# Kernel optimization log

Hardware: AMD Instinct MI355X
Metric: run time of the kernel (lower is better)

The kernel has to match this reference:

```python
import jax, jax.numpy as jnp
import numpy as np

N_CLASSES = 256
N_AUDIO_CHANS = 1
N_CHANS = 128
N_RES = 128
N_SKIP = 256
N_END = 256
KERNEL = 2
N_LAYERS = 10
N_STACKS = 3
DILATIONS = [2 ** i for _ in range(N_STACKS) for i in range(N_LAYERS)]
L = len(DILATIONS)
DN = ('NCW', 'OIW', 'NCW')


def setup_inputs() -> dict:
    key = jax.random.key(0)
    ks = jax.random.split(key, 16)
    s = 0.05  # small init keeps 30-layer residual stack numerically tame
    inp = {
        'x': jax.random.normal(ks[0], (4, N_AUDIO_CHANS, 16384), jnp.float32),
        'w_shift': jax.random.normal(ks[1], (N_CHANS, N_AUDIO_CHANS, KERNEL), jnp.float32) * s,
        'b_shift': jnp.zeros((N_CHANS,), jnp.float32),
        'conv_w': jax.random.normal(ks[2], (L, 2 * N_RES, N_CHANS, KERNEL), jnp.float32) * s,
        'conv_b': jnp.zeros((L, 2 * N_RES), jnp.float32),
        'res_w': jax.random.normal(ks[3], (L, N_CHANS, N_RES), jnp.float32) * s,
        'res_b': jnp.zeros((L, N_CHANS), jnp.float32),
        'skip_w': jax.random.normal(ks[4], (L, N_SKIP, N_RES), jnp.float32) * s,
        'skip_b': jnp.zeros((L, N_SKIP), jnp.float32),
        'a_w': jax.random.normal(ks[5], (N_END, N_SKIP), jnp.float32) * s,
        'a_b': jnp.zeros((N_END,), jnp.float32),
        'b_w': jax.random.normal(ks[6], (N_CLASSES * N_AUDIO_CHANS, N_END), jnp.float32) * s,
        'b_b': jnp.zeros((N_CLASSES * N_AUDIO_CHANS,), jnp.float32),
    }
    return inp


def _causal_conv(x, w, b, dilation):
    # left-pad by (k-1)*dilation so outputs depend only on past/present
    pad = (w.shape[-1] - 1) * dilation
    xp = jnp.pad(x, ((0, 0), (0, 0), (pad, 0)))
    y = jax.lax.conv_general_dilated(xp, w, window_strides=(1,), padding='VALID',
                                     rhs_dilation=(dilation,), dimension_numbers=DN)
    return y + b[None, :, None]


def reference(x, w_shift, b_shift, conv_w, conv_b, res_w, res_b,
              skip_w, skip_b, a_w, a_b, b_w, b_b):
    N, C, W = x.shape
    # shifted conv: shift input right by one (prepend 0, drop last), then causal conv
    xs = jnp.pad(x, ((0, 0), (0, 0), (1, 0)))[:, :, :-1]
    h = _causal_conv(xs, w_shift, b_shift, 1)  # (N, n_chans, W)

    skips = jnp.zeros((N, N_SKIP, W), h.dtype)
    for l in range(L):
        g = _causal_conv(h, conv_w[l], conv_b[l], DILATIONS[l])  # (N, 2*res, W)
        a, b_gate = jnp.split(g, 2, axis=1)
        gated = a * jax.nn.sigmoid(b_gate)                        # GLU, (N, res, W)
        h = jnp.einsum('or,nrw->now', res_w[l], gated) + res_b[l][None, :, None] + h
        skips = skips + jnp.einsum('or,nrw->now', skip_w[l], gated) + skip_b[l][None, :, None]

    z = jax.nn.relu(skips)
    z = jax.nn.relu(jnp.einsum('os,nsw->now', a_w, z) + a_b[None, :, None])
    logits = jnp.einsum('oe,new->now', b_w, z) + b_b[None, :, None]
    return logits.reshape(N, N_CLASSES, N_AUDIO_CHANS, W)
```

## Files before the change

### kernel.cpp

```cpp
#include <hip/hip_runtime.h>
#include <math.h>


#define NB 4
#define WLEN 16384
#define C 128
#define S 256
#define NLAYERS 30
#define TT 64
#define NTB (WLEN / TT)
#define XROW 264
#define GROW 136
#define HW 128

typedef _Float16 half8 __attribute__((ext_vector_type(8)));
typedef _Float16 half4 __attribute__((ext_vector_type(4)));
typedef float floatx4 __attribute__((ext_vector_type(4)));

__device__ __forceinline__ float sigmoidf_(float v) {
    return 1.0f / (1.0f + __expf(-v));
}

__global__ void prep_kernel(const float* __restrict__ conv_w,
                            const float* __restrict__ res_w,
                            const float* __restrict__ skip_w,
                            const float* __restrict__ a_w,
                            const float* __restrict__ b_w,
                            const float* __restrict__ conv_b,
                            const float* __restrict__ skip_b,
                            _Float16* __restrict__ cw,
                            _Float16* __restrict__ rsw,
                            _Float16* __restrict__ skw,
                            _Float16* __restrict__ aw,
                            _Float16* __restrict__ bw,
                            float* __restrict__ cbp,
                            float* __restrict__ ssum) {
    const int ncw = NLAYERS * 256 * 256;
    const int nrs = NLAYERS * 128 * 128;
    const int nsk = NLAYERS * 256 * 128;
    const int nab = 256 * 256;
    const int ncb = NLAYERS * 256;
    const int total = ncw + nrs + nsk + nab + nab + ncb + 256;
    for (int idx = blockIdx.x * blockDim.x + threadIdx.x; idx < total;
         idx += gridDim.x * blockDim.x) {
        int i = idx;
        if (i < ncw) {
            int j = i & 7, lane = (i >> 3) & 63, rest = i >> 9;
            int ks = rest & 7; rest >>= 3;
            int mt = rest & 15; int l = rest >> 4;
            int mp = mt * 16 + (lane & 15);
            int orow = (mp >> 1) + (mp & 1) * 128;
            int k = ks * 32 + (lane >> 4) * 8 + j;
            int tap = k >> 7, c = k & 127;
            cw[i] = (_Float16)conv_w[(((size_t)l * 256 + orow) * 128 + c) * 2 + tap];
        } else if (i < ncw + nrs) {
            i -= ncw;
            int j = i & 7, lane = (i >> 3) & 63, rest = i >> 9;
            int ks = rest & 3; rest >>= 2;
            int mt = rest & 7; int l = rest >> 3;
            int m = mt * 16 + (lane & 15);
            int k = ks * 32 + (lane >> 4) * 8 + j;
            rsw[i] = (_Float16)res_w[((size_t)l * 128 + m) * 128 + k];
        } else if (i < ncw + nrs + nsk) {
            i -= ncw + nrs;
            int j = i & 7, lane = (i >> 3) & 63, rest = i >> 9;
            int ks = rest & 3; rest >>= 2;
            int mt = rest & 15; int l = rest >> 4;
            int m = mt * 16 + (lane & 15);
            int k = ks * 32 + (lane >> 4) * 8 + j;
            skw[i] = (_Float16)skip_w[((size_t)l * 256 + m) * 128 + k];
        } else if (i < ncw + nrs + nsk + nab) {
            i -= ncw + nrs + nsk;
            int j = i & 7, lane = (i >> 3) & 63, rest = i >> 9;
            int ks = rest & 7; int mt = rest >> 3;
            aw[i] = (_Float16)a_w[(mt * 16 + (lane & 15)) * 256 + ks * 32 + (lane >> 4) * 8 + j];
        } else if (i < ncw + nrs + nsk + 2 * nab) {
            i -= ncw + nrs + nsk + nab;
            int j = i & 7, lane = (i >> 3) & 63, rest = i >> 9;
            int ks = rest & 7; int mt = rest >> 3;
            bw[i] = (_Float16)b_w[(mt * 16 + (lane & 15)) * 256 + ks * 32 + (lane >> 4) * 8 + j];
        } else if (i < ncw + nrs + nsk + 2 * nab + ncb) {
            i -= ncw + nrs + nsk + 2 * nab;
            int mp = i & 255; int l = i >> 8;
            cbp[i] = conv_b[l * 256 + (mp >> 1) + (mp & 1) * 128];
        } else {
            i -= ncw + nrs + nsk + 2 * nab + ncb;
            float s = 0.f;
            for (int l = 0; l < NLAYERS; ++l) s += skip_b[l * 256 + i];
            ssum[i] = s;
        }
    }
}

__global__ void front_kernel(const float* __restrict__ x,
                             const float* __restrict__ w_shift,
                             const float* __restrict__ b_shift,
                             _Float16* __restrict__ h) {
    const int n = blockIdx.y;
    const int t = blockIdx.x * 256 + threadIdx.x;
    float x1 = (t >= 1) ? x[n * WLEN + t - 1] : 0.0f;
    float x2 = (t >= 2) ? x[n * WLEN + t - 2] : 0.0f;
    _Float16* hq = h + ((size_t)n * WLEN + t) * 128;
    #pragma unroll
    for (int c0 = 0; c0 < 128; c0 += 8) {
        half8 v;
        #pragma unroll
        for (int j = 0; j < 8; ++j) {
            int c = c0 + j;
            v[j] = (_Float16)fmaf(w_shift[2 * c], x2,
                                  fmaf(w_shift[2 * c + 1], x1, b_shift[c]));
        }
        *(half8*)&hq[c0] = v;
    }
}

template <bool FIRST>
__global__ __launch_bounds__(512, 4) void stack_kernel(
    const _Float16* __restrict__ h_in, _Float16* __restrict__ h_out,
    _Float16* __restrict__ chunk,
    const _Float16* __restrict__ cw0, const float* __restrict__ cb0,
    const _Float16* __restrict__ rsw0, const float* __restrict__ rb0,
    const _Float16* __restrict__ skw0, const float* __restrict__ ssum) {
    __shared__ _Float16 SMEM[2 * HW * GROW];
    _Float16* H = SMEM;
    _Float16* G = SMEM + HW * GROW;
    const int n = blockIdx.y, tb = blockIdx.x, t0 = tb * TT;
    const int tid = threadIdx.x;
    const int wave = __builtin_amdgcn_readfirstlane(tid >> 6);
    const int lane = tid & 63, q = lane >> 4, ml = lane & 15;

    floatx4 sacc[2][4];
    if (FIRST) {
        #pragma unroll
        for (int mt = 0; mt < 2; ++mt)
            #pragma unroll
            for (int r = 0; r < 4; ++r) {
                float bias = ssum[32 * wave + mt * 16 + q * 4 + r];
                #pragma unroll
                for (int nt = 0; nt < 4; ++nt) sacc[mt][nt][r] = bias;
            }
    } else {
        const _Float16* cp = chunk + ((size_t)n * NTB + tb) * 16384;
        #pragma unroll
        for (int mt = 0; mt < 2; ++mt)
            #pragma unroll
            for (int nt = 0; nt < 4; ++nt) {
                size_t o = (size_t)((((wave * 2 + mt) * 4) + nt) * 64 + lane) * 4;
                half4 v = *(const half4*)&cp[o];
                #pragma unroll
                for (int r = 0; r < 4; ++r) sacc[mt][nt][r] = (float)v[r];
            }
    }

    const _Float16* hn = h_in + (size_t)n * WLEN * 128;
    #pragma unroll
    for (int it = 0; it < 4; ++it) {
        int idx = it * 512 + tid;
        int seg = idx & 15;
        int w = idx >> 4;
        int src_t = t0 - 64 + w;
        half8 v = (half8)(_Float16)0.0f;
        if (src_t >= 0)
            v = *(const half8*)&hn[(size_t)src_t * 128 + seg * 8];
        *(half8*)&H[w * GROW + seg * 8] = v;
    }
    __syncthreads();

    const _Float16* cw  = cw0;
    const float*    cb  = cb0;
    const _Float16* rsw = rsw0;
    const float*    rb  = rb0;
    const _Float16* skw = skw0;

    #pragma clang loop unroll(disable)
    for (int j = 0; j < 6; ++j) {
        const int d = 1 << j;

        #pragma unroll
        for (int np = 0; np < 2; ++np) {
            floatx4 acc[2][4];
            #pragma unroll
            for (int mt = 0; mt < 2; ++mt)
                #pragma unroll
                for (int r = 0; r < 4; ++r) {
                    float bias = cb[32 * wave + mt * 16 + q * 4 + r];
                    #pragma unroll
                    for (int nt = 0; nt < 4; ++nt) acc[mt][nt][r] = bias;
                }
            #pragma unroll
            for (int hp = 0; hp < 2; ++hp) {
                for (int ks = 0; ks < 4; ++ks) {
                    half8 a[2];
                    #pragma unroll
                    for (int mt = 0; mt < 2; ++mt)
                        a[mt] = *(const half8*)&cw[((((2 * wave + mt) * 8) + hp * 4 + ks) * 64 + lane) * 8];
                    #pragma unroll
                    for (int nt = 0; nt < 4; ++nt) {
                        int row = np * 64 + nt * 16 + ml;
                        if (!hp) { row -= d; if (row < 0) row = 0; }
                        half8 b = *(const half8*)&H[row * GROW + ks * 32 + q * 8];
                        #pragma unroll
                        for (int mt = 0; mt < 2; ++mt)
                            acc[mt][nt] = __builtin_amdgcn_mfma_f32_16x16x32_f16(a[mt], b, acc[mt][nt], 0, 0, 0);
                    }
                }
            }
            #pragma unroll
            for (int mt = 0; mt < 2; ++mt)
                #pragma unroll
                for (int nt = 0; nt < 4; ++nt) {
                    float g0 = acc[mt][nt][0] * sigmoidf_(acc[mt][nt][1]);
                    float g1 = acc[mt][nt][2] * sigmoidf_(acc[mt][nt][3]);
                    _Float16 p[2] = {(_Float16)g0, (_Float16)g1};
                    *(uint32_t*)&G[(np * 64 + nt * 16 + ml) * GROW + 16 * wave + mt * 8 + 2 * q] = *(uint32_t*)p;
                }
        }
        __syncthreads();

        #pragma unroll
        for (int ks = 0; ks < 4; ++ks) {
            half8 a[2];
            #pragma unroll
            for (int mt = 0; mt < 2; ++mt)
                a[mt] = *(const half8*)&skw[((((2 * wave + mt) * 4) + ks) * 64 + lane) * 8];
            #pragma unroll
            for (int nt = 0; nt < 4; ++nt) {
                half8 b = *(const half8*)&G[(64 + nt * 16 + ml) * GROW + ks * 32 + q * 8];
                #pragma unroll
                for (int mt = 0; mt < 2; ++mt)
                    sacc[mt][nt] = __builtin_amdgcn_mfma_f32_16x16x32_f16(a[mt], b, sacc[mt][nt], 0, 0, 0);
            }
        }

        #pragma unroll
        for (int np = 0; np < 2; ++np) {
            floatx4 racc[4];
            #pragma unroll
            for (int r = 0; r < 4; ++r) {
                float bias = rb[16 * wave + q * 4 + r];
                #pragma unroll
                for (int nt = 0; nt < 4; ++nt) racc[nt][r] = bias;
            }
            #pragma unroll
            for (int ks = 0; ks < 4; ++ks) {
                half8 a = *(const half8*)&rsw[(((wave * 4) + ks) * 64 + lane) * 8];
                #pragma unroll
                for (int nt = 0; nt < 4; ++nt) {
                    half8 b = *(const half8*)&G[(np * 64 + nt * 16 + ml) * GROW + ks * 32 + q * 8];
                    racc[nt] = __builtin_amdgcn_mfma_f32_16x16x32_f16(a, b, racc[nt], 0, 0, 0);
                }
            }
            #pragma unroll
            for (int nt = 0; nt < 4; ++nt) {
                int w = np * 64 + nt * 16 + ml;
                int c = 16 * wave + q * 4;
                half4 hv = *(const half4*)&H[w * GROW + c];
                half4 o;
                #pragma unroll
                for (int r = 0; r < 4; ++r)
                    o[r] = (_Float16)(racc[nt][r] + (float)hv[r]);
                *(half4*)&H[w * GROW + c] = o;
            }
        }
        __syncthreads();

        cw  += 65536; cb += 256; rsw += 16384; rb += 128; skw += 32768;
    }

    _Float16* ho = h_out + (size_t)n * WLEN * 128;
    #pragma unroll
    for (int it = 0; it < 2; ++it) {
        int idx = it * 512 + tid;
        int seg = idx & 15;
        int w64 = idx >> 4;
        *(half8*)&ho[(size_t)(t0 + w64) * 128 + seg * 8] =
            *(const half8*)&H[(64 + w64) * GROW + seg * 8];
    }

    {
        _Float16* cp = chunk + ((size_t)n * NTB + tb) * 16384;
        #pragma unroll
        for (int mt = 0; mt < 2; ++mt)
            #pragma unroll
            for (int nt = 0; nt < 4; ++nt) {
                size_t o = (size_t)((((wave * 2 + mt) * 4) + nt) * 64 + lane) * 4;
                half4 v;
                #pragma unroll
                for (int r = 0; r < 4; ++r) v[r] = (_Float16)sacc[mt][nt][r];
                *(half4*)&cp[o] = v;
            }
    }
}

__global__ __launch_bounds__(512, 8) void layer_kernel(
    const _Float16* __restrict__ h_in, _Float16* __restrict__ h_out,
    _Float16* __restrict__ chunk,
    const _Float16* __restrict__ cw, const float* __restrict__ cb,
    const _Float16* __restrict__ rsw, const float* __restrict__ rb,
    const _Float16* __restrict__ skw, int d) {
    __shared__ _Float16 SMEM[2 * TT * GROW];
    _Float16* X0 = SMEM;
    _Float16* X1 = SMEM + TT * GROW;
    _Float16* G  = X0;
    const int n = blockIdx.y, tb = blockIdx.x, t0 = tb * TT;
    const int tid = threadIdx.x;
    const int wave = __builtin_amdgcn_readfirstlane(tid >> 6);
    const int lane = tid & 63, q = lane >> 4, ml = lane & 15;

    const _Float16* hn = h_in + (size_t)n * WLEN * 128;
    #pragma unroll
    for (int it = 0; it < 4; ++it) {
        int idx = it * 512 + tid;
        int seg = idx & 15;
        int rowc = (idx >> 4) & 63;
        int tap = idx >> 10;
        int src_t = t0 + rowc - (tap ? 0 : d);
        half8 v = (half8)(_Float16)0.0f;
        if (src_t >= 0)
            v = *(const half8*)&hn[(size_t)src_t * 128 + seg * 8];
        _Float16* Xb = tap ? X1 : X0;
        *(half8*)&Xb[rowc * GROW + seg * 8] = v;
    }
    __syncthreads();

    floatx4 acc[2][4];
    #pragma unroll
    for (int mt = 0; mt < 2; ++mt)
        #pragma unroll
        for (int r = 0; r < 4; ++r) {
            float bias = cb[32 * wave + mt * 16 + q * 4 + r];
            #pragma unroll
            for (int nt = 0; nt < 4; ++nt) acc[mt][nt][r] = bias;
        }
    #pragma unroll
    for (int hp = 0; hp < 2; ++hp) {
        const _Float16* Xb = hp ? X1 : X0;
        for (int ks = 0; ks < 4; ++ks) {
            half8 a[2];
            #pragma unroll
            for (int mt = 0; mt < 2; ++mt)
                a[mt] = *(const half8*)&cw[((((2 * wave + mt) * 8) + hp * 4 + ks) * 64 + lane) * 8];
            #pragma unroll
            for (int nt = 0; nt < 4; ++nt) {
                half8 b = *(const half8*)&Xb[(nt * 16 + ml) * GROW + ks * 32 + q * 8];
                #pragma unroll
                for (int mt = 0; mt < 2; ++mt)
                    acc[mt][nt] = __builtin_amdgcn_mfma_f32_16x16x32_f16(a[mt], b, acc[mt][nt], 0, 0, 0);
            }
        }
    }
    __syncthreads();

    #pragma unroll
    for (int mt = 0; mt < 2; ++mt)
        #pragma unroll
        for (int nt = 0; nt < 4; ++nt) {
            float g0 = acc[mt][nt][0] * sigmoidf_(acc[mt][nt][1]);
            float g1 = acc[mt][nt][2] * sigmoidf_(acc[mt][nt][3]);
            _Float16 p[2] = {(_Float16)g0, (_Float16)g1};
            *(uint32_t*)&G[(nt * 16 + ml) * GROW + 16 * wave + mt * 8 + 2 * q] = *(uint32_t*)p;
        }
    __syncthreads();

    {
        floatx4 sacc[2][4];
        #pragma unroll
        for (int mt = 0; mt < 2; ++mt)
            #pragma unroll
            for (int nt = 0; nt < 4; ++nt)
                #pragma unroll
                for (int r = 0; r < 4; ++r) sacc[mt][nt][r] = 0.0f;
        #pragma unroll
        for (int ks = 0; ks < 4; ++ks) {
            half8 a[2];
            #pragma unroll
            for (int mt = 0; mt < 2; ++mt)
                a[mt] = *(const half8*)&skw[((((2 * wave + mt) * 4) + ks) * 64 + lane) * 8];
            #pragma unroll
            for (int nt = 0; nt < 4; ++nt) {
                half8 b = *(const half8*)&G[(nt * 16 + ml) * GROW + ks * 32 + q * 8];
                #pragma unroll
                for (int mt = 0; mt < 2; ++mt)
                    sacc[mt][nt] = __builtin_amdgcn_mfma_f32_16x16x32_f16(a[mt], b, sacc[mt][nt], 0, 0, 0);
            }
        }
        _Float16* cp = chunk + ((size_t)n * NTB + tb) * 16384;
        #pragma unroll
        for (int mt = 0; mt < 2; ++mt)
            #pragma unroll
            for (int nt = 0; nt < 4; ++nt) {
                size_t o = (size_t)((((wave * 2 + mt) * 4) + nt) * 64 + lane) * 4;
                half4 v = *(const half4*)&cp[o];
                half4 w;
                #pragma unroll
                for (int r = 0; r < 4; ++r)
                    w[r] = (_Float16)(sacc[mt][nt][r] + (float)v[r]);
                *(half4*)&cp[o] = w;
            }
    }

    {
        floatx4 racc[4];
        #pragma unroll
        for (int r = 0; r < 4; ++r) {
            float bias = rb[16 * wave + q * 4 + r];
            #pragma unroll
            for (int nt = 0; nt < 4; ++nt) racc[nt][r] = bias;
        }
        #pragma unroll
        for (int ks = 0; ks < 4; ++ks) {
            half8 a = *(const half8*)&rsw[(((wave * 4) + ks) * 64 + lane) * 8];
            #pragma unroll
            for (int nt = 0; nt < 4; ++nt) {
                half8 b = *(const half8*)&G[(nt * 16 + ml) * GROW + ks * 32 + q * 8];
                racc[nt] = __builtin_amdgcn_mfma_f32_16x16x32_f16(a, b, racc[nt], 0, 0, 0);
            }
        }
        _Float16* ho = h_out + (size_t)n * WLEN * 128;
        #pragma unroll
        for (int nt = 0; nt < 4; ++nt) {
            int tt = nt * 16 + ml;
            int c = 16 * wave + q * 4;
            half4 hv = *(const half4*)&X1[tt * GROW + c];
            half4 o;
            #pragma unroll
            for (int r = 0; r < 4; ++r)
                o[r] = (_Float16)(racc[nt][r] + (float)hv[r]);
            *(half4*)&ho[(size_t)(t0 + tt) * 128 + c] = o;
        }
    }
}

__global__ __launch_bounds__(512, 8) void head_kernel(
    float* __restrict__ out, const _Float16* __restrict__ chunk,
    const _Float16* __restrict__ aw, const float* __restrict__ ab,
    const _Float16* __restrict__ bw, const float* __restrict__ bb) {
    __shared__ _Float16 X[TT * XROW];
    const int n = blockIdx.y, tb = blockIdx.x, t0 = tb * TT;
    const int tid = threadIdx.x;
    const int wave = __builtin_amdgcn_readfirstlane(tid >> 6);
    const int lane = tid & 63, q = lane >> 4, ml = lane & 15;

    {
        const _Float16* cp = chunk + ((size_t)n * NTB + tb) * 16384;
        #pragma unroll
        for (int mt = 0; mt < 2; ++mt)
            #pragma unroll
            for (int nt = 0; nt < 4; ++nt) {
                size_t o = (size_t)((((wave * 2 + mt) * 4) + nt) * 64 + lane) * 4;
                half4 v = *(const half4*)&cp[o];
                half4 z;
                #pragma unroll
                for (int r = 0; r < 4; ++r)
                    z[r] = (_Float16)fmaxf((float)v[r], 0.0f);
                *(half4*)&X[(nt * 16 + ml) * XROW + 32 * wave + mt * 16 + q * 4] = z;
            }
    }
    __syncthreads();

    floatx4 acc[2][4];
    #pragma unroll
    for (int mt = 0; mt < 2; ++mt)
        #pragma unroll
        for (int r = 0; r < 4; ++r) {
            float bias = ab[32 * wave + mt * 16 + q * 4 + r];
            #pragma unroll
            for (int nt = 0; nt < 4; ++nt) acc[mt][nt][r] = bias;
        }
    for (int ks = 0; ks < 8; ++ks) {
        half8 a[2];
        #pragma unroll
        for (int mt = 0; mt < 2; ++mt)
            a[mt] = *(const half8*)&aw[((((2 * wave + mt) * 8) + ks) * 64 + lane) * 8];
        #pragma unroll
        for (int nt = 0; nt < 4; ++nt) {
            half8 b = *(const half8*)&X[(nt * 16 + ml) * XROW + ks * 32 + q * 8];
            #pragma unroll
            for (int mt = 0; mt < 2; ++mt)
                acc[mt][nt] = __builtin_amdgcn_mfma_f32_16x16x32_f16(a[mt], b, acc[mt][nt], 0, 0, 0);
        }
    }
    __syncthreads();
    #pragma unroll
    for (int mt = 0; mt < 2; ++mt)
        #pragma unroll
        for (int nt = 0; nt < 4; ++nt) {
            half4 z;
            #pragma unroll
            for (int r = 0; r < 4; ++r)
                z[r] = (_Float16)fmaxf(acc[mt][nt][r], 0.0f);
            *(half4*)&X[(nt * 16 + ml) * XROW + 32 * wave + mt * 16 + q * 4] = z;
        }
    __syncthreads();

    #pragma unroll
    for (int mt = 0; mt < 2; ++mt)
        #pragma unroll
        for (int r = 0; r < 4; ++r) {
            float bias = bb[32 * wave + mt * 16 + q * 4 + r];
            #pragma unroll
            for (int nt = 0; nt < 4; ++nt) acc[mt][nt][r] = bias;
        }
    for (int ks = 0; ks < 8; ++ks) {
        half8 a[2];
        #pragma unroll
        for (int mt = 0; mt < 2; ++mt)
            a[mt] = *(const half8*)&bw[((((2 * wave + mt) * 8) + ks) * 64 + lane) * 8];
        #pragma unroll
        for (int nt = 0; nt < 4; ++nt) {
            half8 b = *(const half8*)&X[(nt * 16 + ml) * XROW + ks * 32 + q * 8];
            #pragma unroll
            for (int mt = 0; mt < 2; ++mt)
                acc[mt][nt] = __builtin_amdgcn_mfma_f32_16x16x32_f16(a[mt], b, acc[mt][nt], 0, 0, 0);
        }
    }
    float* on = out + (size_t)n * S * WLEN;
    #pragma unroll
    for (int mt = 0; mt < 2; ++mt)
        #pragma unroll
        for (int nt = 0; nt < 4; ++nt)
            #pragma unroll
            for (int r = 0; r < 4; ++r) {
                int o = 32 * wave + mt * 16 + q * 4 + r;
                int tt = t0 + nt * 16 + ml;
                on[(size_t)o * WLEN + tt] = acc[mt][nt][r];
            }
}

extern "C" void kernel_launch(void* const* d_in, const int* in_sizes, int n_in,
                              void* d_out, int out_size, void* d_ws, size_t ws_size,
                              hipStream_t stream) {
    (void)in_sizes; (void)n_in; (void)out_size; (void)ws_size;
    const float* x       = (const float*)d_in[0];
    const float* w_shift = (const float*)d_in[1];
    const float* b_shift = (const float*)d_in[2];
    const float* conv_w  = (const float*)d_in[3];
    const float* conv_b  = (const float*)d_in[4];
    const float* res_w   = (const float*)d_in[5];
    const float* res_b   = (const float*)d_in[6];
    const float* skip_w  = (const float*)d_in[7];
    const float* skip_b  = (const float*)d_in[8];
    const float* a_w     = (const float*)d_in[9];
    const float* a_b     = (const float*)d_in[10];
    const float* b_w     = (const float*)d_in[11];
    const float* b_b     = (const float*)d_in[12];
    float* out = (float*)d_out;

    char* ws = (char*)d_ws;
    size_t off = 0;
    _Float16* hA    = (_Float16*)(ws + off); off += (size_t)NB * WLEN * 128 * 2;
    _Float16* hB    = (_Float16*)(ws + off); off += (size_t)NB * WLEN * 128 * 2;
    _Float16* chunk = (_Float16*)(ws + off); off += (size_t)NB * NTB * 16384 * 2;
    _Float16* cw  = (_Float16*)(ws + off); off += (size_t)NLAYERS * 256 * 256 * 2;
    _Float16* rsw = (_Float16*)(ws + off); off += (size_t)NLAYERS * 128 * 128 * 2;
    _Float16* skw = (_Float16*)(ws + off); off += (size_t)NLAYERS * 256 * 128 * 2;
    _Float16* aw  = (_Float16*)(ws + off); off += 256 * 256 * 2;
    _Float16* bw  = (_Float16*)(ws + off); off += 256 * 256 * 2;
    float* cbp  = (float*)(ws + off); off += (size_t)NLAYERS * 256 * 4;
    float* ssum = (float*)(ws + off); off += 256 * 4;

    prep_kernel<<<512, 256, 0, stream>>>(conv_w, res_w, skip_w, a_w, b_w,
                                         conv_b, skip_b,
                                         cw, rsw, skw, aw, bw, cbp, ssum);
    front_kernel<<<dim3(WLEN / 256, NB), 256, 0, stream>>>(x, w_shift, b_shift, hA);

    const dim3 grid(NTB, NB);
    _Float16* hin = hA;
    _Float16* hout = hB;
    for (int s = 0; s < 3; ++s) {
        const int l0 = s * 10;
        if (s == 0)
            stack_kernel<true><<<grid, 512, 0, stream>>>(
                hin, hout, chunk,
                cw + (size_t)l0 * 65536, cbp + l0 * 256,
                rsw + (size_t)l0 * 16384, res_b + l0 * 128,
                skw + (size_t)l0 * 32768, ssum);
        else
            stack_kernel<false><<<grid, 512, 0, stream>>>(
                hin, hout, chunk,
                cw + (size_t)l0 * 65536, cbp + l0 * 256,
                rsw + (size_t)l0 * 16384, res_b + l0 * 128,
                skw + (size_t)l0 * 32768, ssum);
        { _Float16* tmp = hin; hin = hout; hout = tmp; }
        for (int jj = 6; jj < 10; ++jj) {
            const int l = l0 + jj;
            const int dil = 1 << jj;
            layer_kernel<<<grid, 512, 0, stream>>>(
                hin, hout, chunk,
                cw + (size_t)l * 65536, cbp + l * 256,
                rsw + (size_t)l * 16384, res_b + l * 128,
                skw + (size_t)l * 32768, dil);
            _Float16* tmp = hin; hin = hout; hout = tmp;
        }
    }

    head_kernel<<<grid, 512, 0, stream>>>(out, chunk, aw, a_b, bw, b_b);
}
```

Baseline: 1.099 ms.

## Split fused stack kernel into two with tight halos and XOR-swizzled LDS

The fused first-six-layer kernel is split into two templated kernels. One runs layers with dilations 1–8 using a 16-step halo; the other runs dilations 16–32 using a 48-step halo. Both replace the old uniform 64-step halo, which cut redundant recomputation of overlap rows per tile. LDS rows are now XOR-swizzled instead of padded, and launch bounds are raised so smaller shared-memory tiles allow more resident blocks. In exchange there is an extra kernel launch plus one more round trip of the hidden state and skip chunk through global memory.

```diff
diff --git a/kernel.cpp b/kernel.cpp
--- a/kernel.cpp
+++ b/kernel.cpp
@@ -11,7 +11,8 @@
 #define NTB (WLEN / TT)
 #define XROW 264
 #define GROW 136
-#define HW 128
+
+#define SX(row, c) ((row) * 128 + ((c) ^ (((row) & 7) << 3)))
 
 typedef _Float16 half8 __attribute__((ext_vector_type(8)));
 typedef _Float16 half4 __attribute__((ext_vector_type(4)));
@@ -114,16 +115,17 @@
     }
 }
 
-template <bool FIRST>
-__global__ __launch_bounds__(512, 4) void stack_kernel(
+template <int E0, int NL, int NT, int HALO, bool FIRST>
+__global__ __launch_bounds__(512, 8) void stack_kernel(
     const _Float16* __restrict__ h_in, _Float16* __restrict__ h_out,
     _Float16* __restrict__ chunk,
     const _Float16* __restrict__ cw0, const float* __restrict__ cb0,
     const _Float16* __restrict__ rsw0, const float* __restrict__ rb0,
     const _Float16* __restrict__ skw0, const float* __restrict__ ssum) {
-    __shared__ _Float16 SMEM[2 * HW * GROW];
+    constexpr int WR = NT * 16;
+    __shared__ _Float16 SMEM[2 * WR * 128];
     _Float16* H = SMEM;
-    _Float16* G = SMEM + HW * GROW;
+    _Float16* G = SMEM + WR * 128;
     const int n = blockIdx.y, tb = blockIdx.x, t0 = tb * TT;
     const int tid = threadIdx.x;
     const int wave = __builtin_amdgcn_readfirstlane(tid >> 6);
@@ -154,15 +156,17 @@
 
     const _Float16* hn = h_in + (size_t)n * WLEN * 128;
     #pragma unroll
-    for (int it = 0; it < 4; ++it) {
+    for (int it = 0; it < (WR * 16 + 511) / 512; ++it) {
         int idx = it * 512 + tid;
-        int seg = idx & 15;
-        int w = idx >> 4;
-        int src_t = t0 - 64 + w;
-        half8 v = (half8)(_Float16)0.0f;
-        if (src_t >= 0)
-            v = *(const half8*)&hn[(size_t)src_t * 128 + seg * 8];
-        *(half8*)&H[w * GROW + seg * 8] = v;
+        if (idx < WR * 16) {
+            int seg = idx & 15;
+            int w = idx >> 4;
+            int src_t = t0 - HALO + w;
+            half8 v = (half8)(_Float16)0.0f;
+            if (src_t >= 0)
+                v = *(const half8*)&hn[(size_t)src_t * 128 + seg * 8];
+            *(half8*)&H[SX(w, seg * 8)] = v;
+        }
     }
     __syncthreads();
 
@@ -173,11 +177,11 @@
     const _Float16* skw = skw0;
 
     #pragma clang loop unroll(disable)
-    for (int j = 0; j < 6; ++j) {
-        const int d = 1 << j;
-
-        #pragma unroll
-        for (int np = 0; np < 2; ++np) {
+    for (int j = 0; j < NL; ++j) {
+        const int d = 1 << (E0 + j);
+
+        #pragma unroll
+        for (int base = 0; base < NT; base += 4) {
             floatx4 acc[2][4];
             #pragma unroll
             for (int mt = 0; mt < 2; ++mt)
@@ -196,12 +200,14 @@
                         a[mt] = *(const half8*)&cw[((((2 * wave + mt) * 8) + hp * 4 + ks) * 64 + lane) * 8];
                     #pragma unroll
                     for (int nt = 0; nt < 4; ++nt) {
-                        int row = np * 64 + nt * 16 + ml;
-                        if (!hp) { row -= d; if (row < 0) row = 0; }
-                        half8 b = *(const half8*)&H[row * GROW + ks * 32 + q * 8];
-                        #pragma unroll
-                        for (int mt = 0; mt < 2; ++mt)
-                            acc[mt][nt] = __builtin_amdgcn_mfma_f32_16x16x32_f16(a[mt], b, acc[mt][nt], 0, 0, 0);
+                        if (base + nt < NT) {
+                            int row = (base + nt) * 16 + ml;
+                            if (!hp) { row -= d; if (row < 0) row = 0; }
+                            half8 b = *(const half8*)&H[SX(row, ks * 32 + q * 8)];
+                            #pragma unroll
+                            for (int mt = 0; mt < 2; ++mt)
+                                acc[mt][nt] = __builtin_amdgcn_mfma_f32_16x16x32_f16(a[mt], b, acc[mt][nt], 0, 0, 0);
+                        }
                     }
                 }
             }
@@ -209,10 +215,12 @@
             for (int mt = 0; mt < 2; ++mt)
                 #pragma unroll
                 for (int nt = 0; nt < 4; ++nt) {
-                    float g0 = acc[mt][nt][0] * sigmoidf_(acc[mt][nt][1]);
-                    float g1 = acc[mt][nt][2] * sigmoidf_(acc[mt][nt][3]);
-                    _Float16 p[2] = {(_Float16)g0, (_Float16)g1};
-                    *(uint32_t*)&G[(np * 64 + nt * 16 + ml) * GROW + 16 * wave + mt * 8 + 2 * q] = *(uint32_t*)p;
+                    if (base + nt < NT) {
+                        float g0 = acc[mt][nt][0] * sigmoidf_(acc[mt][nt][1]);
+                        float g1 = acc[mt][nt][2] * sigmoidf_(acc[mt][nt][3]);
+                        _Float16 p[2] = {(_Float16)g0, (_Float16)g1};
+                        *(uint32_t*)&G[SX((base + nt) * 16 + ml, 16 * wave + mt * 8 + 2 * q)] = *(uint32_t*)p;
+                    }
                 }
         }
         __syncthreads();
@@ -225,7 +233,7 @@
                 a[mt] = *(const half8*)&skw[((((2 * wave + mt) * 4) + ks) * 64 + lane) * 8];
             #pragma unroll
             for (int nt = 0; nt < 4; ++nt) {
-                half8 b = *(const half8*)&G[(64 + nt * 16 + ml) * GROW + ks * 32 + q * 8];
+                half8 b = *(const half8*)&G[SX(HALO + nt * 16 + ml, ks * 32 + q * 8)];
                 #pragma unroll
                 for (int mt = 0; mt < 2; ++mt)
                     sacc[mt][nt] = __builtin_amdgcn_mfma_f32_16x16x32_f16(a[mt], b, sacc[mt][nt], 0, 0, 0);
@@ -233,7 +241,7 @@
         }
 
         #pragma unroll
-        for (int np = 0; np < 2; ++np) {
+        for (int base = 0; base < NT; base += 4) {
             floatx4 racc[4];
             #pragma unroll
             for (int r = 0; r < 4; ++r) {
@@ -246,20 +254,24 @@
                 half8 a = *(const half8*)&rsw[(((wave * 4) + ks) * 64 + lane) * 8];
                 #pragma unroll
                 for (int nt = 0; nt < 4; ++nt) {
-                    half8 b = *(const half8*)&G[(np * 64 + nt * 16 + ml) * GROW + ks * 32 + q * 8];
-                    racc[nt] = __builtin_amdgcn_mfma_f32_16x16x32_f16(a, b, racc[nt], 0, 0, 0);
+                    if (base + nt < NT) {
+                        half8 b = *(const half8*)&G[SX((base + nt) * 16 + ml, ks * 32 + q * 8)];
+                        racc[nt] = __builtin_amdgcn_mfma_f32_16x16x32_f16(a, b, racc[nt], 0, 0, 0);
+                    }
                 }
             }
             #pragma unroll
             for (int nt = 0; nt < 4; ++nt) {
-                int w = np * 64 + nt * 16 + ml;
-                int c = 16 * wave + q * 4;
-                half4 hv = *(const half4*)&H[w * GROW + c];
-                half4 o;
-                #pragma unroll
-                for (int r = 0; r < 4; ++r)
-                    o[r] = (_Float16)(racc[nt][r] + (float)hv[r]);
-                *(half4*)&H[w * GROW + c] = o;
+                if (base + nt < NT) {
+                    int w = (base + nt) * 16 + ml;
+                    int c = 16 * wave + q * 4;
+                    half4 hv = *(const half4*)&H[SX(w, c)];
+                    half4 o;
+                    #pragma unroll
+                    for (int r = 0; r < 4; ++r)
+                        o[r] = (_Float16)(racc[nt][r] + (float)hv[r]);
+                    *(half4*)&H[SX(w, c)] = o;
+                }
             }
         }
         __syncthreads();
@@ -274,7 +286,7 @@
         int seg = idx & 15;
         int w64 = idx >> 4;
         *(half8*)&ho[(size_t)(t0 + w64) * 128 + seg * 8] =
-            *(const half8*)&H[(64 + w64) * GROW + seg * 8];
+            *(const half8*)&H[SX(HALO + w64, seg * 8)];
     }
 
     {
@@ -570,18 +582,27 @@
     for (int s = 0; s < 3; ++s) {
         const int l0 = s * 10;
         if (s == 0)
-            stack_kernel<true><<<grid, 512, 0, stream>>>(
+            stack_kernel<0, 4, 5, 16, true><<<grid, 512, 0, stream>>>(
                 hin, hout, chunk,
                 cw + (size_t)l0 * 65536, cbp + l0 * 256,
                 rsw + (size_t)l0 * 16384, res_b + l0 * 128,
                 skw + (size_t)l0 * 32768, ssum);
         else
-            stack_kernel<false><<<grid, 512, 0, stream>>>(
+            stack_kernel<0, 4, 5, 16, false><<<grid, 512, 0, stream>>>(
                 hin, hout, chunk,
                 cw + (size_t)l0 * 65536, cbp + l0 * 256,
                 rsw + (size_t)l0 * 16384, res_b + l0 * 128,
                 skw + (size_t)l0 * 32768, ssum);
         { _Float16* tmp = hin; hin = hout; hout = tmp; }
+        {
+            const int lb = l0 + 4;
+            stack_kernel<4, 2, 7, 48, false><<<grid, 512, 0, stream>>>(
+                hin, hout, chunk,
+                cw + (size_t)lb * 65536, cbp + lb * 256,
+                rsw + (size_t)lb * 16384, res_b + lb * 128,
+                skw + (size_t)lb * 32768, ssum);
+            _Float16* tmp = hin; hin = hout; hout = tmp;
+        }
         for (int jj = 6; jj < 10; ++jj) {
             const int l = l0 + jj;
             const int dil = 1 << jj;
```

Result: slower. 2.697 ms (+145.4%).
